# Performance work log

Measured on AMD Instinct MI355X. Metric: run time of the kernel, lower is better.

Reference implementation:

```python
import jax, jax.numpy as jnp
import numpy as np

B, C, H, W = 8, 512, 64, 64
D = C // 8  # 64

def setup_inputs() -> dict:
    key = jax.random.key(0)
    ks = jax.random.split(key, 10)
    s = 0.02
    return {
        "x":  jax.random.normal(ks[0], (B, C, H, W), dtype=jnp.float32),
        "Wq": jax.random.normal(ks[1], (D, C), dtype=jnp.float32) * s,
        "bq": jnp.zeros((D,), dtype=jnp.float32),
        "Wk": jax.random.normal(ks[2], (D, C), dtype=jnp.float32) * s,
        "bk": jnp.zeros((D,), dtype=jnp.float32),
        "Wv": jax.random.normal(ks[3], (D, C), dtype=jnp.float32) * s,
        "bv": jnp.zeros((D,), dtype=jnp.float32),
        "Wo": jax.random.normal(ks[4], (C, D), dtype=jnp.float32) * s,
        "bo": jnp.zeros((C,), dtype=jnp.float32),
        "gamma": jnp.full((1,), 0.5, dtype=jnp.float32),
    }

def reference(x, Wq, bq, Wk, bk, Wv, bv, Wo, bo, gamma):
    b, c, h, w = x.shape
    n = h * w
    xf = x.reshape(b, c, n)                                   # (B, C, N)
    # 1x1 convs == channel matmuls (spectral_norm only reparametrizes the weight)
    q = jnp.einsum('dc,bcn->bnd', Wq, xf) + bq                # (B, N, D)
    k = jnp.einsum('dc,bcn->bdn', Wk, xf) + bk[:, None]       # (B, D, N)
    v = jnp.einsum('dc,bcn->bdn', Wv, xf) + bv[:, None]       # (B, D, N)
    # unscaled scores, softmax over key index (last dim)
    attn = jax.nn.softmax(jnp.einsum('bnd,bdm->bnm', q, k), axis=-1)  # (B, N, N)
    out = jnp.einsum('bdm,bnm->bdn', v, attn)                 # (B, D, N)
    out = jnp.einsum('cd,bdn->bcn', Wo, out) + bo[:, None]    # (B, C, N)
    return (out * gamma + xf).reshape(b, c, h, w)
```

## Files before the change

kernel.cpp:

```cpp
#include <hip/hip_runtime.h>
#include <hip/hip_bf16.h>

#define DEVFN __device__ __forceinline__

typedef __bf16 bf16x8 __attribute__((ext_vector_type(8)));
typedef float f32x4 __attribute__((ext_vector_type(4)));
typedef float float4_t __attribute__((ext_vector_type(4)));
typedef unsigned short ushort8_t __attribute__((ext_vector_type(8)));
typedef unsigned short ushort4_t __attribute__((ext_vector_type(4)));
typedef unsigned int uint4_t __attribute__((ext_vector_type(4)));

constexpr int Bd = 8, Cd = 512, Nd = 4096, Dd = 64;

DEVFN unsigned short f2bf(float f) {
    union { float f; unsigned int u; } v; v.f = f;
    unsigned int r = (v.u + 0x7FFFu + ((v.u >> 16) & 1u)) >> 16;
    return (unsigned short)r;
}

DEVFN unsigned int pack2(float a, float b) {
    __hip_bfloat162 h = __float22bfloat162_rn(make_float2(a, b));
    union { __hip_bfloat162 h; unsigned int u; } c; c.h = h;
    return c.u;
}

DEVFN bf16x8 ld_bf8(const unsigned short* p) {
    ushort8_t u = *(const ushort8_t*)p;
    return __builtin_bit_cast(bf16x8, u);
}

DEVFN f32x4 mfma16(bf16x8 a, bf16x8 b, f32x4 c) {
    return __builtin_amdgcn_mfma_f32_16x16x32_bf16(a, b, c, 0, 0, 0);
}

__global__ __launch_bounds__(256) void k_cvtw(
    const float* __restrict__ Wq, const float* __restrict__ Wk,
    const float* __restrict__ Wv, const float* __restrict__ Wo,
    unsigned short* __restrict__ w4)
{
    int i = blockIdx.x * 256 + threadIdx.x;
    w4[i]          = f2bf(Wq[i]);
    w4[32768 + i]  = f2bf(Wk[i]);
    w4[65536 + i]  = f2bf(Wv[i]);
    w4[98304 + i]  = f2bf(Wo[i]);
}

__global__ __launch_bounds__(256, 2) void k_qkv(
    const float* __restrict__ x,
    const unsigned short* __restrict__ wq,
    const unsigned short* __restrict__ wk,
    const unsigned short* __restrict__ wv,
    const float* __restrict__ bq, const float* __restrict__ bk, const float* __restrict__ bv,
    unsigned short* __restrict__ q_nd, unsigned short* __restrict__ k_nd,
    unsigned short* __restrict__ v_dn)
{
    const int b   = blockIdx.y;
    const int n0  = blockIdx.x * 64;
    const int tid = threadIdx.x, wid = tid >> 6, l = tid & 63;
    const int lo  = l & 15, hi = l >> 4;
    const float* xb = x + (size_t)b * Cd * Nd + n0;

    __shared__ __align__(16) unsigned short sm[512 * 64];

    const int lr = tid >> 4;
    const int nc = (tid & 15) * 4;
    #pragma unroll
    for (int half = 0; half < 2; ++half) {
        float4_t xr[16];
        #pragma unroll
        for (int r = 0; r < 16; ++r) {
            const int c = half * 256 + r * 16 + lr;
            xr[r] = *(const float4_t*)(xb + (size_t)c * Nd + nc);
        }
        __builtin_amdgcn_sched_barrier(0);
        #pragma unroll
        for (int r = 0; r < 16; ++r) {
            const int c = half * 256 + r * 16 + lr;
            const int s = ((c >> 3) & 3) << 4;
            ushort4_t u;
            #pragma unroll
            for (int j = 0; j < 4; ++j) u[j] = f2bf(xr[r][j]);
            *(ushort4_t*)&sm[c * 64 + (nc ^ s)] = u;
        }
    }
    __syncthreads();

    f32x4 acc[12] = {};
    for (int t = 0; t < 8; ++t) {
        #pragma unroll
        for (int kk = 0; kk < 2; ++kk) {
            const int cbase = t * 64 + kk * 32 + hi * 8;
            const int s   = ((cbase >> 3) & 3) << 4;
            const int col = (wid * 16 + lo) ^ s;
            ushort8_t ua;
            #pragma unroll
            for (int j = 0; j < 8; ++j)
                ua[j] = sm[(cbase + j) * 64 + col];
            bf16x8 af = __builtin_bit_cast(bf16x8, ua);
            #pragma unroll
            for (int jj = 0; jj < 12; ++jj) {
                const unsigned short* wm = (jj < 4) ? wq : (jj < 8) ? wk : wv;
                const int d0 = (jj & 3) * 16;
                bf16x8 bf = ld_bf8(wm + (d0 + lo) * Cd + t * 64 + kk * 32 + hi * 8);
                acc[jj] = mfma16(af, bf, acc[jj]);
            }
        }
    }
    __syncthreads();

    unsigned short* tl = sm + wid * (16 * 72);
    #pragma unroll
    for (int m = 0; m < 2; ++m) {
        const float* bias = m ? bk : bq;
        #pragma unroll
        for (int jj = 0; jj < 4; ++jj) {
            const float bia = bias[jj * 16 + lo];
            #pragma unroll
            for (int r = 0; r < 4; ++r)
                tl[(hi * 4 + r) * 72 + jj * 16 + lo] = f2bf(acc[m * 4 + jj][r] + bia);
        }
        asm volatile("" ::: "memory");
        const int row = l >> 2, dg = l & 3;
        ushort8_t a0 = *(const ushort8_t*)&tl[row * 72 + dg * 16];
        ushort8_t a1 = *(const ushort8_t*)&tl[row * 72 + dg * 16 + 8];
        unsigned short* dst = (m ? k_nd : q_nd)
            + ((size_t)b * Nd + n0 + wid * 16 + row) * 64 + dg * 16;
        *(ushort8_t*)dst = a0; *(ushort8_t*)(dst + 8) = a1;
        asm volatile("" ::: "memory");
    }
    __syncthreads();

    unsigned short* vt = sm;
    #pragma unroll
    for (int jj = 0; jj < 4; ++jj) {
        const float bia = bv[jj * 16 + lo];
        #pragma unroll
        for (int r = 0; r < 4; ++r)
            vt[(jj * 16 + lo) * 72 + wid * 16 + hi * 4 + r] = f2bf(acc[8 + jj][r] + bia);
    }
    __syncthreads();
    {
        const int d = tid >> 2, ng = tid & 3;
        ushort8_t a0 = *(const ushort8_t*)&vt[d * 72 + ng * 16];
        ushort8_t a1 = *(const ushort8_t*)&vt[d * 72 + ng * 16 + 8];
        unsigned short* dst = v_dn + ((size_t)b * Dd + d) * Nd + n0 + ng * 16;
        *(ushort8_t*)dst = a0; *(ushort8_t*)(dst + 8) = a1;
    }
}

__global__ __launch_bounds__(512, 4) void k_attn(
    const unsigned short* __restrict__ q_nd,
    const unsigned short* __restrict__ k_nd,
    const unsigned short* __restrict__ v_dn,
    unsigned short* __restrict__ o_nd)
{
    const int bid = blockIdx.x;
    const int b   = bid & 7;
    const int n0  = (bid >> 3) * 64;
    const int tid = threadIdx.x, wid = tid >> 6, l = tid & 63;
    const int lo  = l & 15, hi = l >> 4;
    const int lsw = lo & 7;
    const int qh  = wid >> 2;
    const int kh  = (wid >> 1) & 1;
    const int tp  = wid & 1;
    const int wk0 = kh * 32;

    __shared__ __align__(16) unsigned short kv_lds[2][2][2][64 * 64];
    __shared__ float red_l[3][2][2][16];

    const unsigned short* qb = q_nd + (size_t)b * Nd * Dd;
    const unsigned short* kb = k_nd + (size_t)b * Nd * Dd;
    const unsigned short* vb = v_dn + (size_t)b * Dd * Nd;

    bf16x8 aq[2][2];
    #pragma unroll
    for (int qs = 0; qs < 2; ++qs)
        #pragma unroll
        for (int kc = 0; kc < 2; ++kc)
            aq[qs][kc] = ld_bf8(qb + (size_t)(n0 + qh*32 + qs*16 + lo) * 64 + kc*32 + hi*8);

    f32x4 acc[2][4] = {};
    float l_p[2] = {0.f, 0.f};

    const int sr = tid >> 3, ss = tid & 7;
    const int kwsl = (ss ^ (sr & 7)) * 8;
    const int vkh = ss >> 2, vsl = ss & 3, vms = vsl >> 1;
    const int vg0 = vkh * 4 + ((2 * vsl) & 3);
    const int vg1 = vkh * 4 + ((2 * vsl + 1) & 3);
    const int vsw = sr & 7;
    ushort8_t kr0, kr1, vr0, vr1;

    auto gload = [&](int it) {
        const size_t m1 = (size_t)it * 128;
        kr0 = *(const ushort8_t*)(kb + (m1 + sr) * 64 + ss * 8);
        kr1 = *(const ushort8_t*)(kb + (m1 + 64 + sr) * 64 + ss * 8);
        vr0 = *(const ushort8_t*)(vb + (size_t)sr * Nd + m1 + ss * 8);
        vr1 = *(const ushort8_t*)(vb + (size_t)sr * Nd + m1 + 64 + ss * 8);
    };
    auto dswrite = [&](int buf) {
        unsigned short* kt0 = &kv_lds[0][buf][0][0];
        unsigned short* kt1 = &kv_lds[0][buf][1][0];
        unsigned short* vt0 = &kv_lds[1][buf][0][0];
        unsigned short* vt1 = &kv_lds[1][buf][1][0];
        *(ushort8_t*)(kt0 + sr * 64 + kwsl) = kr0;
        *(ushort8_t*)(kt1 + sr * 64 + kwsl) = kr1;
        ushort4_t a0 = __builtin_shufflevector(vr0, vr0, 0, 1, 2, 3);
        ushort4_t a1 = __builtin_shufflevector(vr0, vr0, 4, 5, 6, 7);
        ushort4_t b0 = __builtin_shufflevector(vr1, vr1, 0, 1, 2, 3);
        ushort4_t b1 = __builtin_shufflevector(vr1, vr1, 4, 5, 6, 7);
        *(ushort4_t*)(vt0 + sr * 64 + (vg0 ^ vsw) * 8 + vms * 4) = a0;
        *(ushort4_t*)(vt0 + sr * 64 + (vg1 ^ vsw) * 8 + vms * 4) = a1;
        *(ushort4_t*)(vt1 + sr * 64 + (vg0 ^ vsw) * 8 + vms * 4) = b0;
        *(ushort4_t*)(vt1 + sr * 64 + (vg1 ^ vsw) * 8 + vms * 4) = b1;
    };

    auto compute = [&](int buf) {
        const unsigned short* kt = &kv_lds[0][buf][tp][0];
        const unsigned short* vt = &kv_lds[1][buf][tp][0];
        f32x4 s[2][2] = {};
        #pragma unroll
        for (int ms = 0; ms < 2; ++ms) {
            #pragma unroll
            for (int kc = 0; kc < 2; ++kc) {
                bf16x8 kf = ld_bf8(kt + (wk0 + ms*16 + lo) * 64 + (((kc*4 + hi) ^ lsw) * 8));
                #pragma unroll
                for (int qs = 0; qs < 2; ++qs)
                    s[qs][ms] = mfma16(kf, aq[qs][kc], s[qs][ms]);
            }
        }
        bf16x8 vf[4];
        #pragma unroll
        for (int ds = 0; ds < 4; ++ds)
            vf[ds] = ld_bf8(vt + (ds*16 + lo) * 64 + (((kh*4 + hi) ^ lsw) * 8));
        #pragma unroll
        for (int qs = 0; qs < 2; ++qs) {
            float p[2][4];
            #pragma unroll
            for (int ms = 0; ms < 2; ++ms)
                #pragma unroll
                for (int r = 0; r < 4; ++r)
                    p[ms][r] = __expf(s[qs][ms][r]);
            l_p[qs] += ((p[0][0] + p[0][1]) + (p[0][2] + p[0][3]))
                     + ((p[1][0] + p[1][1]) + (p[1][2] + p[1][3]));
            uint4_t w;
            w[0] = pack2(p[0][0], p[0][1]);
            w[1] = pack2(p[0][2], p[0][3]);
            w[2] = pack2(p[1][0], p[1][1]);
            w[3] = pack2(p[1][2], p[1][3]);
            bf16x8 apf = __builtin_bit_cast(bf16x8, w);
            #pragma unroll
            for (int ds = 0; ds < 4; ++ds)
                acc[qs][ds] = mfma16(apf, vf[ds], acc[qs][ds]);
        }
    };

    constexpr int NIT = Nd / 128;
    gload(0);
    dswrite(0);
    __syncthreads();
    for (int it = 0; it < NIT; ++it) {
        const int cur = it & 1;
        if (it + 1 < NIT) gload(it + 1);
        __builtin_amdgcn_sched_barrier(0);
        compute(cur);
        if (it + 1 < NIT) dswrite(cur ^ 1);
        __syncthreads();
    }

    float lh[2];
    #pragma unroll
    for (int qs = 0; qs < 2; ++qs) {
        float ps = l_p[qs];
        ps += __shfl_xor(ps, 16, 64);
        ps += __shfl_xor(ps, 32, 64);
        lh[qs] = ps;
    }
    float* red = (float*)&kv_lds[0][0][0][0];
    const int g = (kh * 2 + tp) - 1;
    if (g >= 0) {
        #pragma unroll
        for (int qs = 0; qs < 2; ++qs) {
            #pragma unroll
            for (int ds = 0; ds < 4; ++ds) {
                const int idx = ((g * 2 + qh) * 2 + qs) * 4 + ds;
                *(f32x4*)&red[idx * 256 + l * 4] = acc[qs][ds];
            }
            red_l[g][qh][qs][lo] = lh[qs];
        }
    }
    __syncthreads();
    if (g < 0) {
        #pragma unroll
        for (int qs = 0; qs < 2; ++qs) {
            #pragma unroll
            for (int gg = 0; gg < 3; ++gg) {
                #pragma unroll
                for (int ds = 0; ds < 4; ++ds) {
                    const int idx = ((gg * 2 + qh) * 2 + qs) * 4 + ds;
                    acc[qs][ds] += *(const f32x4*)&red[idx * 256 + l * 4];
                }
                lh[qs] += red_l[gg][qh][qs][lo];
            }
            #pragma unroll
            for (int r = 0; r < 4; ++r) {
                float lq = __shfl(lh[qs], hi * 4 + r, 16);
                float rl = 1.0f / lq;
                #pragma unroll
                for (int ds = 0; ds < 4; ++ds) {
                    float o = acc[qs][ds][r] * rl;
                    o_nd[((size_t)b * Nd + n0 + qh*32 + qs*16 + hi*4 + r) * 64 + ds*16 + lo] = f2bf(o);
                }
            }
        }
    }
}

__global__ __launch_bounds__(256) void k_oproj(
    const unsigned short* __restrict__ o_nd,
    const unsigned short* __restrict__ wo,
    const float* __restrict__ bo,
    const float* __restrict__ gamma,
    const float* __restrict__ x,
    float* __restrict__ out)
{
    const int b   = blockIdx.y;
    const int n0  = blockIdx.x * 64;
    const int tid = threadIdx.x, wid = tid >> 6, l = tid & 63;
    const int lo  = l & 15, hi = l >> 4;
    const int n0w = n0 + wid * 16;
    const float g = gamma[0];

    bf16x8 ao[2];
    #pragma unroll
    for (int kc = 0; kc < 2; ++kc)
        ao[kc] = ld_bf8(o_nd + ((size_t)b * Nd + n0w + lo) * 64 + kc*32 + hi*8);

    for (int ct = 0; ct < 32; ++ct) {
        f32x4 acc = {};
        #pragma unroll
        for (int kc = 0; kc < 2; ++kc) {
            bf16x8 bw = ld_bf8(wo + (ct*16 + lo) * 64 + kc*32 + hi*8);
            acc = mfma16(ao[kc], bw, acc);
        }
        const int c = ct*16 + lo;
        const float bc = bo[c];
        const size_t base = ((size_t)b * Cd + c) * Nd + n0w + hi*4;
        float4_t xv = *(const float4_t*)(x + base);
        float4_t ov;
        #pragma unroll
        for (int r = 0; r < 4; ++r) ov[r] = g * (acc[r] + bc) + xv[r];
        *(float4_t*)(out + base) = ov;
    }
}

extern "C" void kernel_launch(void* const* d_in, const int* in_sizes, int n_in,
                              void* d_out, int out_size, void* d_ws, size_t ws_size,
                              hipStream_t stream) {
    (void)in_sizes; (void)n_in; (void)out_size; (void)ws_size;
    const float* x  = (const float*)d_in[0];
    const float* Wq = (const float*)d_in[1];
    const float* bq = (const float*)d_in[2];
    const float* Wk = (const float*)d_in[3];
    const float* bk = (const float*)d_in[4];
    const float* Wv = (const float*)d_in[5];
    const float* bv = (const float*)d_in[6];
    const float* Wo = (const float*)d_in[7];
    const float* bo = (const float*)d_in[8];
    const float* gm = (const float*)d_in[9];
    float* out = (float*)d_out;

    unsigned short* w4   = (unsigned short*)d_ws;
    unsigned short* q_nd = w4 + 131072;
    unsigned short* k_nd = q_nd + (size_t)Bd * Nd * Dd;
    unsigned short* v_dn = k_nd + (size_t)Bd * Nd * Dd;
    unsigned short* o_nd = v_dn + (size_t)Bd * Nd * Dd;

    k_cvtw<<<128, 256, 0, stream>>>(Wq, Wk, Wv, Wo, w4);
    dim3 gq(Nd / 64, Bd);
    k_qkv<<<gq, 256, 0, stream>>>(x, w4, w4 + 32768, w4 + 65536, bq, bk, bv, q_nd, k_nd, v_dn);
    k_attn<<<512, 512, 0, stream>>>(q_nd, k_nd, v_dn, o_nd);
    dim3 g1(Nd / 64, Bd);
    k_oproj<<<g1, 256, 0, stream>>>(o_nd, w4 + 98304, bo, gm, x, out);
}
```

Before: 141.9 us.

## Double query rows per attention block to reuse each K/V tile across 128 queries

Each attention block now processes 128 query rows instead of 64, so every wave holds four 16-row query subtiles, and the grid shrinks from 512 to 256 blocks. This halves the global and LDS traffic for K/V tiles per query and doubles the MFMA work per LDS fragment load. To fit the larger fp32 accumulators into the reused LDS space, the cross-wave reduction now runs in two stages with extra barriers. Launch bounds drop to one block per CU, which allows more registers but leaves 256 blocks on the MI355X's 256 CUs, so latency hiding depends on a single block per CU.

```diff
diff --git a/kernel.cpp b/kernel.cpp
--- a/kernel.cpp
+++ b/kernel.cpp
@@ -148,7 +148,7 @@
     }
 }
 
-__global__ __launch_bounds__(512, 4) void k_attn(
+__global__ __launch_bounds__(512, 1) void k_attn(
     const unsigned short* __restrict__ q_nd,
     const unsigned short* __restrict__ k_nd,
     const unsigned short* __restrict__ v_dn,
@@ -156,7 +156,7 @@
 {
     const int bid = blockIdx.x;
     const int b   = bid & 7;
-    const int n0  = (bid >> 3) * 64;
+    const int n0  = (bid >> 3) * 128;
     const int tid = threadIdx.x, wid = tid >> 6, l = tid & 63;
     const int lo  = l & 15, hi = l >> 4;
     const int lsw = lo & 7;
@@ -166,21 +166,21 @@
     const int wk0 = kh * 32;
 
     __shared__ __align__(16) unsigned short kv_lds[2][2][2][64 * 64];
-    __shared__ float red_l[3][2][2][16];
+    __shared__ float red_l[2][2][4][16];
 
     const unsigned short* qb = q_nd + (size_t)b * Nd * Dd;
     const unsigned short* kb = k_nd + (size_t)b * Nd * Dd;
     const unsigned short* vb = v_dn + (size_t)b * Dd * Nd;
 
-    bf16x8 aq[2][2];
-    #pragma unroll
-    for (int qs = 0; qs < 2; ++qs)
+    bf16x8 aq[4][2];
+    #pragma unroll
+    for (int qs = 0; qs < 4; ++qs)
         #pragma unroll
         for (int kc = 0; kc < 2; ++kc)
-            aq[qs][kc] = ld_bf8(qb + (size_t)(n0 + qh*32 + qs*16 + lo) * 64 + kc*32 + hi*8);
-
-    f32x4 acc[2][4] = {};
-    float l_p[2] = {0.f, 0.f};
+            aq[qs][kc] = ld_bf8(qb + (size_t)(n0 + qh*64 + qs*16 + lo) * 64 + kc*32 + hi*8);
+
+    f32x4 acc[4][4] = {};
+    float l_p[4] = {0.f, 0.f, 0.f, 0.f};
 
     const int sr = tid >> 3, ss = tid & 7;
     const int kwsl = (ss ^ (sr & 7)) * 8;
@@ -217,14 +217,14 @@
     auto compute = [&](int buf) {
         const unsigned short* kt = &kv_lds[0][buf][tp][0];
         const unsigned short* vt = &kv_lds[1][buf][tp][0];
-        f32x4 s[2][2] = {};
+        f32x4 s[4][2] = {};
         #pragma unroll
         for (int ms = 0; ms < 2; ++ms) {
             #pragma unroll
             for (int kc = 0; kc < 2; ++kc) {
                 bf16x8 kf = ld_bf8(kt + (wk0 + ms*16 + lo) * 64 + (((kc*4 + hi) ^ lsw) * 8));
                 #pragma unroll
-                for (int qs = 0; qs < 2; ++qs)
+                for (int qs = 0; qs < 4; ++qs)
                     s[qs][ms] = mfma16(kf, aq[qs][kc], s[qs][ms]);
             }
         }
@@ -233,7 +233,7 @@
         for (int ds = 0; ds < 4; ++ds)
             vf[ds] = ld_bf8(vt + (ds*16 + lo) * 64 + (((kh*4 + hi) ^ lsw) * 8));
         #pragma unroll
-        for (int qs = 0; qs < 2; ++qs) {
+        for (int qs = 0; qs < 4; ++qs) {
             float p[2][4];
             #pragma unroll
             for (int ms = 0; ms < 2; ++ms)
@@ -267,40 +267,65 @@
         __syncthreads();
     }
 
-    float lh[2];
-    #pragma unroll
-    for (int qs = 0; qs < 2; ++qs) {
+    float lh[4];
+    #pragma unroll
+    for (int qs = 0; qs < 4; ++qs) {
         float ps = l_p[qs];
         ps += __shfl_xor(ps, 16, 64);
         ps += __shfl_xor(ps, 32, 64);
         lh[qs] = ps;
     }
     float* red = (float*)&kv_lds[0][0][0][0];
-    const int g = (kh * 2 + tp) - 1;
-    if (g >= 0) {
-        #pragma unroll
-        for (int qs = 0; qs < 2; ++qs) {
+    const int g = kh * 2 + tp;
+    if (g == 1 || g == 2) {
+        const int slot = g - 1;
+        #pragma unroll
+        for (int qs = 0; qs < 4; ++qs) {
             #pragma unroll
             for (int ds = 0; ds < 4; ++ds) {
-                const int idx = ((g * 2 + qh) * 2 + qs) * 4 + ds;
+                const int idx = ((slot * 2 + qh) * 4 + qs) * 4 + ds;
                 *(f32x4*)&red[idx * 256 + l * 4] = acc[qs][ds];
             }
-            red_l[g][qh][qs][lo] = lh[qs];
-        }
-    }
-    __syncthreads();
-    if (g < 0) {
-        #pragma unroll
-        for (int qs = 0; qs < 2; ++qs) {
-            #pragma unroll
-            for (int gg = 0; gg < 3; ++gg) {
+            red_l[slot][qh][qs][lo] = lh[qs];
+        }
+    }
+    __syncthreads();
+    if (g == 0) {
+        #pragma unroll
+        for (int slot = 0; slot < 2; ++slot) {
+            #pragma unroll
+            for (int qs = 0; qs < 4; ++qs) {
                 #pragma unroll
                 for (int ds = 0; ds < 4; ++ds) {
-                    const int idx = ((gg * 2 + qh) * 2 + qs) * 4 + ds;
+                    const int idx = ((slot * 2 + qh) * 4 + qs) * 4 + ds;
                     acc[qs][ds] += *(const f32x4*)&red[idx * 256 + l * 4];
                 }
-                lh[qs] += red_l[gg][qh][qs][lo];
-            }
+                lh[qs] += red_l[slot][qh][qs][lo];
+            }
+        }
+    }
+    __syncthreads();
+    if (g == 3) {
+        #pragma unroll
+        for (int qs = 0; qs < 4; ++qs) {
+            #pragma unroll
+            for (int ds = 0; ds < 4; ++ds) {
+                const int idx = ((0 * 2 + qh) * 4 + qs) * 4 + ds;
+                *(f32x4*)&red[idx * 256 + l * 4] = acc[qs][ds];
+            }
+            red_l[0][qh][qs][lo] = lh[qs];
+        }
+    }
+    __syncthreads();
+    if (g == 0) {
+        #pragma unroll
+        for (int qs = 0; qs < 4; ++qs) {
+            #pragma unroll
+            for (int ds = 0; ds < 4; ++ds) {
+                const int idx = ((0 * 2 + qh) * 4 + qs) * 4 + ds;
+                acc[qs][ds] += *(const f32x4*)&red[idx * 256 + l * 4];
+            }
+            lh[qs] += red_l[0][qh][qs][lo];
             #pragma unroll
             for (int r = 0; r < 4; ++r) {
                 float lq = __shfl(lh[qs], hi * 4 + r, 16);
@@ -308,7 +333,7 @@
                 #pragma unroll
                 for (int ds = 0; ds < 4; ++ds) {
                     float o = acc[qs][ds][r] * rl;
-                    o_nd[((size_t)b * Nd + n0 + qh*32 + qs*16 + hi*4 + r) * 64 + ds*16 + lo] = f2bf(o);
+                    o_nd[((size_t)b * Nd + n0 + qh*64 + qs*16 + hi*4 + r) * 64 + ds*16 + lo] = f2bf(o);
                 }
             }
         }
@@ -378,7 +403,7 @@
     k_cvtw<<<128, 256, 0, stream>>>(Wq, Wk, Wv, Wo, w4);
     dim3 gq(Nd / 64, Bd);
     k_qkv<<<gq, 256, 0, stream>>>(x, w4, w4 + 32768, w4 + 65536, bq, bk, bv, q_nd, k_nd, v_dn);
-    k_attn<<<512, 512, 0, stream>>>(q_nd, k_nd, v_dn, o_nd);
+    k_attn<<<256, 512, 0, stream>>>(q_nd, k_nd, v_dn, o_nd);
     dim3 g1(Nd / 64, Bd);
     k_oproj<<<g1, 256, 0, stream>>>(o_nd, w4 + 98304, bo, gm, x, out);
 }
```

New measurement: 142.9 us. No clear change (+0.7%).
